# Performance work log

Measured on AMD Instinct MI355X. Metric: run time of the kernel, lower is better.

## Reference

```python
import jax, jax.numpy as jnp
import numpy as np

N, IN_DIM, HEADS, C = 100000, 128, 4, 32  # out_dim = HEADS*C = 128
E = 1600000


def setup_inputs() -> dict:
    key = jax.random.key(0)
    ks = jax.random.split(key, 9)
    x = jax.random.normal(ks[0], (N, IN_DIM), dtype=jnp.float32)
    edge_index = jax.random.randint(ks[1], (2, E), 0, N, dtype=jnp.int64)
    # GATConv params
    W = jax.random.normal(ks[2], (HEADS * C, IN_DIM), dtype=jnp.float32) * (1.0 / np.sqrt(IN_DIM))
    att_src = jax.random.normal(ks[3], (HEADS, C), dtype=jnp.float32) * 0.1
    att_dst = jax.random.normal(ks[4], (HEADS, C), dtype=jnp.float32) * 0.1
    bias = jax.random.normal(ks[5], (HEADS * C,), dtype=jnp.float32) * 0.01
    # complex phase + LayerNorm params
    phase = jax.random.normal(ks[6], (HEADS * C,), dtype=jnp.float32) * 0.02
    gamma = 1.0 + jax.random.normal(ks[7], (HEADS * C,), dtype=jnp.float32) * 0.01
    beta = jax.random.normal(ks[8], (HEADS * C,), dtype=jnp.float32) * 0.01
    return {"x": x, "edge_index": edge_index, "W": W, "att_src": att_src,
            "att_dst": att_dst, "bias": bias, "phase": phase, "gamma": gamma, "beta": beta}


def reference(x, edge_index, W, att_src, att_dst, bias, phase, gamma, beta):
    src, dst = edge_index[0], edge_index[1]
    h = (x @ W.T).reshape(N, HEADS, C)                      # [N,H,C]
    a_src = jnp.einsum('nhc,hc->nh', h, att_src)            # [N,H]
    a_dst = jnp.einsum('nhc,hc->nh', h, att_dst)
    e = jax.nn.leaky_relu(a_src[src] + a_dst[dst], 0.2)     # [E,H]
    # segment softmax over destination nodes (numerically stable)
    m = jax.ops.segment_max(e, dst, num_segments=N)         # [N,H]
    ex = jnp.exp(e - m[dst])
    s = jax.ops.segment_sum(ex, dst, num_segments=N)        # [N,H]
    alpha = ex / (s[dst] + 1e-16)                           # [E,H]
    msg = h[src] * alpha[:, :, None]                        # [E,H,C]
    out = jax.ops.segment_sum(msg, dst, num_segments=N).reshape(N, HEADS * C) + bias
    # complex phase magnitude: sqrt((h cos p)^2 + (h sin p)^2 + eps)
    mag = jnp.sqrt((out * jnp.cos(phase)) ** 2 + (out * jnp.sin(phase)) ** 2 + 1e-12)
    # LayerNorm
    mu = mag.mean(-1, keepdims=True)
    var = ((mag - mu) ** 2).mean(-1, keepdims=True)
    hn = (mag - mu) / jnp.sqrt(var + 1e-5) * gamma + beta
    return jax.nn.gelu(hn, approximate=False)
```

## Files before the change

kernel.cpp:

```cpp
#include <hip/hip_runtime.h>
#include <hip/hip_bf16.h>

#define N_ 100000
#define E_ 1600000
#define D_ 128
#define H_ 4
#define C_ 32
#define XSTR 136
#define NSCAT 256
#define E_CHUNK 6250
#define PARTS 782
#define NP 128
#define EBUF 2560
#define NLIN 512
#define FLAT (PARTS * NSCAT)
#define SCB 196

using bf16 = __hip_bfloat16;
typedef __attribute__((ext_vector_type(8))) short short8;
typedef __attribute__((ext_vector_type(4))) float f32x4;
typedef __attribute__((ext_vector_type(2))) float f32x2;

__device__ __forceinline__ float u2f(unsigned u) { return __uint_as_float(u); }
__device__ __forceinline__ unsigned short f2bu(float v) {
  bf16 t = __float2bfloat16(v);
  return *(unsigned short*)&t;
}

__global__ __launch_bounds__(256) void k_linear_histo(
    const float* __restrict__ x, const float* __restrict__ W,
    const float* __restrict__ att_src, const float* __restrict__ att_dst,
    const int* __restrict__ ei, int* __restrict__ count,
    bf16* __restrict__ h, float* __restrict__ a_src, float* __restrict__ a_dst) {
  __shared__ unsigned short WB[16384];
  __shared__ unsigned short XS[64 * XSTR];
  __shared__ float ats[128], atd[128];
  const int tid = threadIdx.x;
  const int bid = blockIdx.x;

  if (bid >= NLIN) {
    int* hist = (int*)WB;
    const int b = bid - NLIN;
    for (int i = tid; i < PARTS; i += 256) hist[i] = 0;
    __syncthreads();
    const int base = b * E_CHUNK;
    for (int i = tid; i < E_CHUNK; i += 256)
      atomicAdd(&hist[ei[E_ + base + i] >> 7], 1);
    __syncthreads();
    for (int p = tid; p < PARTS; p += 256) count[p * NSCAT + b] = hist[p];
    return;
  }

  const int lb = bid;
  const int lane = tid & 63, w = tid >> 6;
  const int n15 = lane & 15, quad = lane >> 4;

  for (int i = tid; i < 16384; i += 256) {
    const int n = i >> 7, k = i & 127;
    const int kk = k >> 5, q = (k >> 3) & 3, j = k & 7;
    const int frag = kk * 8 + (n >> 4);
    WB[frag * 512 + q * 128 + (n & 15) * 8 + j] = f2bu(W[n * 128 + k]);
  }
  if (tid < 128) { ats[tid] = att_src[tid]; atd[tid] = att_dst[tid]; }
  __syncthreads();

  const int nrb = (N_ + 63) / 64;
  for (int rb = lb; rb < nrb; rb += NLIN) {
    const int row0 = rb * 64;
    const int arow = row0 + w * 16 + n15;

    short8 af[4];
#pragma unroll
    for (int kk = 0; kk < 4; kk++) {
      float4 p = make_float4(0.f, 0.f, 0.f, 0.f);
      float4 q = make_float4(0.f, 0.f, 0.f, 0.f);
      if (arow < N_) {
        const float* xp = &x[(size_t)arow * 128 + kk * 32 + quad * 8];
        p = *(const float4*)xp;
        q = *(const float4*)(xp + 4);
      }
      short8 a;
      a[0] = f2bu(p.x); a[1] = f2bu(p.y); a[2] = f2bu(p.z); a[3] = f2bu(p.w);
      a[4] = f2bu(q.x); a[5] = f2bu(q.y); a[6] = f2bu(q.z); a[7] = f2bu(q.w);
      af[kk] = a;
    }

    f32x4 acc[8] = {};
#pragma unroll
    for (int kk = 0; kk < 4; kk++)
#pragma unroll
      for (int t = 0; t < 8; t++) {
        const short8 bfr = *(const short8*)&WB[(kk * 8 + t) * 512 + lane * 8];
        acc[t] = __builtin_amdgcn_mfma_f32_16x16x32_bf16(af[kk], bfr, acc[t], 0, 0, 0);
      }

#pragma unroll
    for (int t = 0; t < 8; t++)
#pragma unroll
      for (int reg = 0; reg < 4; reg++)
        XS[(w * 16 + quad * 4 + reg) * XSTR + t * 16 + n15] = f2bu(acc[t][reg]);

    const int lrow = lane >> 2, hd = lane & 3, cb = hd * 32;
    const int grow = row0 + w * 16 + lrow;
    if (grow < N_) {
      float ps = 0.f, pd = 0.f;
#pragma unroll
      for (int g = 0; g < 4; g++) {
        const uint4 v = *(const uint4*)&XS[(w * 16 + lrow) * XSTR + cb + g * 8];
        *(uint4*)&h[(size_t)grow * 128 + cb + g * 8] = v;
        const unsigned uu[4] = {v.x, v.y, v.z, v.w};
#pragma unroll
        for (int p2 = 0; p2 < 4; p2++) {
          const float f0 = u2f(uu[p2] << 16);
          const float f1 = u2f(uu[p2] & 0xffff0000u);
          const int cc = cb + g * 8 + p2 * 2;
          ps = fmaf(f0, ats[cc], ps);  ps = fmaf(f1, ats[cc + 1], ps);
          pd = fmaf(f0, atd[cc], pd);  pd = fmaf(f1, atd[cc + 1], pd);
        }
      }
      a_src[grow * 4 + hd] = ps;
      a_dst[grow * 4 + hd] = pd;
    }
  }
}

__global__ __launch_bounds__(1024) void k_scanA(int* __restrict__ count,
                                                int* __restrict__ bsum) {
  __shared__ int ps[1024];
  const int g = blockIdx.x, t = threadIdx.x;
  const int idx = g * 1024 + t;
  const int v = (idx < FLAT) ? count[idx] : 0;
  ps[t] = v;
  __syncthreads();
  for (int off = 1; off < 1024; off <<= 1) {
    const int add = (t >= off) ? ps[t - off] : 0;
    __syncthreads();
    ps[t] += add;
    __syncthreads();
  }
  if (idx < FLAT) count[idx] = ps[t] - v;
  if (t == 1023) bsum[g] = ps[t];
}

__global__ __launch_bounds__(1024) void k_scanB(int* __restrict__ count,
                                                const int* __restrict__ bsum,
                                                int* __restrict__ part_ptr) {
  const int g = blockIdx.x, t = threadIdx.x;
  int off = 0;
  for (int i = 0; i < g; i++) off += bsum[i];
  const int idx = g * 1024 + t;
  if (idx < FLAT) {
    const int val = count[idx] + off;
    count[idx] = val;
    if ((idx & (NSCAT - 1)) == 0) part_ptr[idx / NSCAT] = val;
  }
  if (g == SCB - 1 && t == 1023) part_ptr[PARTS] = E_;
}

__global__ __launch_bounds__(256) void k_scatter(const int* __restrict__ ei,
                                                 const int* __restrict__ base,
                                                 int* __restrict__ eout) {
  __shared__ int lbase[PARTS];
  const int b = blockIdx.x, tid = threadIdx.x;
  for (int p = tid; p < PARTS; p += 256) lbase[p] = base[p * NSCAT + b];
  __syncthreads();
  const int ebase = b * E_CHUNK;
  for (int i = tid; i < E_CHUNK; i += 256) {
    const int e = ebase + i;
    const int s = ei[e];
    const int d = ei[E_ + e];
    const int pos = atomicAdd(&lbase[d >> 7], 1);
    eout[pos] = s | ((d & 127) << 20);
  }
}

__global__ __launch_bounds__(256) void k_sortw(
    const int* __restrict__ part_ptr, int* __restrict__ eout,
    const float* __restrict__ a_src, const float* __restrict__ a_dst,
    float* __restrict__ ew, int* __restrict__ nodeptr, int* __restrict__ degN) {
  __shared__ int ebuf[EBUF];
  __shared__ int lsrc[EBUF];
  __shared__ int lcnt[NP], loff[NP], lptr[NP], ls[NP];
  const int p = blockIdx.x, tid = threadIdx.x;
  const int lo = part_ptr[p];
  int ne = part_ptr[p + 1] - lo;
  if (ne > EBUF) ne = EBUF;

  for (int i = tid; i < ne; i += 256) ebuf[i] = eout[lo + i];
  for (int n = tid; n < NP; n += 256) { lcnt[n] = 0; loff[n] = 0; }
  __syncthreads();
  for (int i = tid; i < ne; i += 256) atomicAdd(&lcnt[ebuf[i] >> 20], 1);
  __syncthreads();
  if (tid < NP) ls[tid] = lcnt[tid];
  __syncthreads();
  for (int off = 1; off < NP; off <<= 1) {
    const int v = (tid < NP && tid >= off) ? ls[tid - off] : 0;
    __syncthreads();
    if (tid < NP) ls[tid] += v;
    __syncthreads();
  }
  if (tid < NP) lptr[tid] = ls[tid] - lcnt[tid];
  __syncthreads();
  for (int i = tid; i < ne; i += 256) {
    const int v = ebuf[i];
    const int n = v >> 20;
    const int s = v & 0x1FFFF;
    const int off = atomicAdd(&loff[n], 1);
    const int pos = lptr[n] + off;
    lsrc[pos] = s;
    const int d = p * NP + n;
    const float4 asv = *(const float4*)&a_src[s * 4];
    const float4 adv = *(const float4*)&a_dst[d * 4];
    float e0 = asv.x + adv.x; e0 = (e0 > 0.f) ? e0 : 0.2f * e0;
    float e1 = asv.y + adv.y; e1 = (e1 > 0.f) ? e1 : 0.2f * e1;
    float e2 = asv.z + adv.z; e2 = (e2 > 0.f) ? e2 : 0.2f * e2;
    float e3 = asv.w + adv.w; e3 = (e3 > 0.f) ? e3 : 0.2f * e3;
    float4 wv;
    wv.x = __expf(e0); wv.y = __expf(e1); wv.z = __expf(e2); wv.w = __expf(e3);
    *(float4*)&ew[(size_t)(lo + pos) * 4] = wv;
  }
  __syncthreads();
  for (int i = tid; i < ne; i += 256) eout[lo + i] = lsrc[i];
  if (tid < NP) {
    const int g = p * NP + tid;
    if (g < N_) { nodeptr[g] = lo + lptr[tid]; degN[g] = lcnt[tid]; }
  }
}

__global__ __launch_bounds__(256) void k_gather(
    const int* __restrict__ nodeptr, const int* __restrict__ degN,
    const int* __restrict__ srcsorted, const float* __restrict__ ew,
    const bf16* __restrict__ h, const float* __restrict__ bias,
    const float* __restrict__ gamma, const float* __restrict__ beta,
    float* __restrict__ out) {
  const int lane = threadIdx.x & 63;
  const int d = blockIdx.x * 4 + (threadIdx.x >> 6);
  if (d >= N_) return;
  const int head = lane >> 4;
  const int ch = lane * 2;
  const int deg0 = degN[d];
  const int deg = deg0 < 64 ? deg0 : 64;
  const int ptr = nodeptr[d];
  const float* __restrict__ ewp = ew + (size_t)ptr * 4;

  int my_src = 0;
  if (lane < deg) my_src = srcsorted[ptr + lane];

  float acc0 = 0.f, acc1 = 0.f, sumw = 0.f;

  int j = 0;
  for (; j + 4 <= deg; j += 4) {
    const int s0 = __builtin_amdgcn_readlane(my_src, j);
    const int s1 = __builtin_amdgcn_readlane(my_src, j + 1);
    const int s2 = __builtin_amdgcn_readlane(my_src, j + 2);
    const int s3 = __builtin_amdgcn_readlane(my_src, j + 3);
    const float w0 = ewp[(j + 0) * 4 + head];
    const float w1 = ewp[(j + 1) * 4 + head];
    const float w2 = ewp[(j + 2) * 4 + head];
    const float w3 = ewp[(j + 3) * 4 + head];
    const unsigned h0 = *(const unsigned*)&h[((size_t)s0 << 7) + ch];
    const unsigned h1 = *(const unsigned*)&h[((size_t)s1 << 7) + ch];
    const unsigned h2 = *(const unsigned*)&h[((size_t)s2 << 7) + ch];
    const unsigned h3 = *(const unsigned*)&h[((size_t)s3 << 7) + ch];
    sumw += w0 + w1 + w2 + w3;
    acc0 = fmaf(w0, u2f(h0 << 16), acc0); acc1 = fmaf(w0, u2f(h0 & 0xffff0000u), acc1);
    acc0 = fmaf(w1, u2f(h1 << 16), acc0); acc1 = fmaf(w1, u2f(h1 & 0xffff0000u), acc1);
    acc0 = fmaf(w2, u2f(h2 << 16), acc0); acc1 = fmaf(w2, u2f(h2 & 0xffff0000u), acc1);
    acc0 = fmaf(w3, u2f(h3 << 16), acc0); acc1 = fmaf(w3, u2f(h3 & 0xffff0000u), acc1);
  }
  for (; j < deg; ++j) {
    const int s = __builtin_amdgcn_readlane(my_src, j);
    const float wv = ewp[j * 4 + head];
    const unsigned hv = *(const unsigned*)&h[((size_t)s << 7) + ch];
    sumw += wv;
    acc0 = fmaf(wv, u2f(hv << 16), acc0);
    acc1 = fmaf(wv, u2f(hv & 0xffff0000u), acc1);
  }

  const float inv = 1.0f / (sumw + 1e-16f);
  const float2 bi = *(const float2*)&bias[ch];
  const float v0 = acc0 * inv + bi.x;
  const float v1 = acc1 * inv + bi.y;
  const float m0i = sqrtf(v0 * v0 + 1e-12f);
  const float m1i = sqrtf(v1 * v1 + 1e-12f);

  float s1r = m0i + m1i;
#pragma unroll
  for (int off = 32; off > 0; off >>= 1) s1r += __shfl_xor(s1r, off);
  const float mu = s1r * (1.0f / 128.0f);
  const float d0 = m0i - mu, d1 = m1i - mu;
  float q = d0 * d0 + d1 * d1;
#pragma unroll
  for (int off = 32; off > 0; off >>= 1) q += __shfl_xor(q, off);
  const float rstd = rsqrtf(q * (1.0f / 128.0f) + 1e-5f);
  const float2 ga = *(const float2*)&gamma[ch];
  const float2 be = *(const float2*)&beta[ch];
  const float hn0 = d0 * rstd * ga.x + be.x;
  const float hn1 = d1 * rstd * ga.y + be.y;
  const float g0 = 0.5f * hn0 * (1.0f + erff(hn0 * 0.70710678118654752f));
  const float g1 = 0.5f * hn1 * (1.0f + erff(hn1 * 0.70710678118654752f));
  f32x2 gv; gv.x = g0; gv.y = g1;
  __builtin_nontemporal_store(gv, (f32x2*)&out[(size_t)d * 128 + ch]);
}

extern "C" void kernel_launch(void* const* d_in, const int* in_sizes, int n_in,
                              void* d_out, int out_size, void* d_ws, size_t ws_size,
                              hipStream_t stream) {
  const float* x       = (const float*)d_in[0];
  const int*   ei      = (const int*)d_in[1];
  const float* W       = (const float*)d_in[2];
  const float* att_src = (const float*)d_in[3];
  const float* att_dst = (const float*)d_in[4];
  const float* bias    = (const float*)d_in[5];
  const float* gamma   = (const float*)d_in[7];
  const float* beta    = (const float*)d_in[8];
  float* out = (float*)d_out;

  bf16*  h        = (bf16*)d_ws;
  float* a_src    = (float*)(h + (size_t)N_ * D_);
  float* a_dst    = a_src + (size_t)N_ * H_;
  int*   count    = (int*)(a_dst + (size_t)N_ * H_);
  int*   bsum     = count + (size_t)FLAT;
  int*   part_ptr = bsum + 256;
  int*   eout     = part_ptr + 800;
  float* ew       = (float*)(eout + (size_t)E_);
  int*   nodeptr  = (int*)(ew + (size_t)E_ * 4);
  int*   degN     = nodeptr + (size_t)N_;

  k_linear_histo<<<NLIN + NSCAT, 256, 0, stream>>>(x, W, att_src, att_dst, ei,
                                                   count, h, a_src, a_dst);
  k_scanA<<<SCB, 1024, 0, stream>>>(count, bsum);
  k_scanB<<<SCB, 1024, 0, stream>>>(count, bsum, part_ptr);
  k_scatter<<<NSCAT, 256, 0, stream>>>(ei, count, eout);
  k_sortw<<<PARTS, 256, 0, stream>>>(part_ptr, eout, a_src, a_dst, ew,
                                     nodeptr, degN);
  k_gather<<<(N_ + 3) / 4, 256, 0, stream>>>(nodeptr, degN, eout, ew, h,
                                             bias, gamma, beta, out);
}
```

Before: 279.7 us.

## Split linear projection across histogram, scan and scatter kernels to overlap work

The dense x@W projection was previously done entirely alongside the histogram kernel. It is now split into four row ranges, each run by extra blocks inside the histogram, scanA, scanB and scatter launches, so the small sort-preparation kernels share the machine with matmul work. The scan kernels also move from 1024-thread blocks to 256-thread blocks that each handle 4 elements. The cost is that every launch now reserves the large shared-memory footprint and reloads W into shared memory, and the load balance depends on the chosen row split.

```diff
diff --git a/kernel.cpp b/kernel.cpp
--- a/kernel.cpp
+++ b/kernel.cpp
@@ -12,9 +12,12 @@
 #define PARTS 782
 #define NP 128
 #define EBUF 2560
-#define NLIN 512
 #define FLAT (PARTS * NSCAT)
-#define SCB 196
+#define NSC 196
+#define RB1 300
+#define RB2 400
+#define RB3 500
+#define NRB 1563
 
 using bf16 = __hip_bfloat16;
 typedef __attribute__((ext_vector_type(8))) short short8;
@@ -27,31 +30,12 @@
   return *(unsigned short*)&t;
 }
 
-__global__ __launch_bounds__(256) void k_linear_histo(
+__device__ __forceinline__ void linear_body(
+    unsigned short* WB, unsigned short* XS, float* ats, float* atd,
     const float* __restrict__ x, const float* __restrict__ W,
     const float* __restrict__ att_src, const float* __restrict__ att_dst,
-    const int* __restrict__ ei, int* __restrict__ count,
-    bf16* __restrict__ h, float* __restrict__ a_src, float* __restrict__ a_dst) {
-  __shared__ unsigned short WB[16384];
-  __shared__ unsigned short XS[64 * XSTR];
-  __shared__ float ats[128], atd[128];
-  const int tid = threadIdx.x;
-  const int bid = blockIdx.x;
-
-  if (bid >= NLIN) {
-    int* hist = (int*)WB;
-    const int b = bid - NLIN;
-    for (int i = tid; i < PARTS; i += 256) hist[i] = 0;
-    __syncthreads();
-    const int base = b * E_CHUNK;
-    for (int i = tid; i < E_CHUNK; i += 256)
-      atomicAdd(&hist[ei[E_ + base + i] >> 7], 1);
-    __syncthreads();
-    for (int p = tid; p < PARTS; p += 256) count[p * NSCAT + b] = hist[p];
-    return;
-  }
-
-  const int lb = bid;
+    bf16* __restrict__ h, float* __restrict__ a_src, float* __restrict__ a_dst,
+    int lb, int nlin, int rb0, int rb1, int tid) {
   const int lane = tid & 63, w = tid >> 6;
   const int n15 = lane & 15, quad = lane >> 4;
 
@@ -64,8 +48,7 @@
   if (tid < 128) { ats[tid] = att_src[tid]; atd[tid] = att_dst[tid]; }
   __syncthreads();
 
-  const int nrb = (N_ + 63) / 64;
-  for (int rb = lb; rb < nrb; rb += NLIN) {
+  for (int rb = rb0 + lb; rb < rb1; rb += nlin) {
     const int row0 = rb * 64;
     const int arow = row0 + w * 16 + n15;
 
@@ -124,54 +107,128 @@
   }
 }
 
-__global__ __launch_bounds__(1024) void k_scanA(int* __restrict__ count,
-                                                int* __restrict__ bsum) {
-  __shared__ int ps[1024];
-  const int g = blockIdx.x, t = threadIdx.x;
-  const int idx = g * 1024 + t;
-  const int v = (idx < FLAT) ? count[idx] : 0;
-  ps[t] = v;
-  __syncthreads();
-  for (int off = 1; off < 1024; off <<= 1) {
-    const int add = (t >= off) ? ps[t - off] : 0;
-    __syncthreads();
-    ps[t] += add;
-    __syncthreads();
-  }
-  if (idx < FLAT) count[idx] = ps[t] - v;
-  if (t == 1023) bsum[g] = ps[t];
-}
-
-__global__ __launch_bounds__(1024) void k_scanB(int* __restrict__ count,
-                                                const int* __restrict__ bsum,
-                                                int* __restrict__ part_ptr) {
-  const int g = blockIdx.x, t = threadIdx.x;
-  int off = 0;
-  for (int i = 0; i < g; i++) off += bsum[i];
-  const int idx = g * 1024 + t;
-  if (idx < FLAT) {
-    const int val = count[idx] + off;
-    count[idx] = val;
-    if ((idx & (NSCAT - 1)) == 0) part_ptr[idx / NSCAT] = val;
-  }
-  if (g == SCB - 1 && t == 1023) part_ptr[PARTS] = E_;
-}
-
-__global__ __launch_bounds__(256) void k_scatter(const int* __restrict__ ei,
-                                                 const int* __restrict__ base,
-                                                 int* __restrict__ eout) {
-  __shared__ int lbase[PARTS];
-  const int b = blockIdx.x, tid = threadIdx.x;
-  for (int p = tid; p < PARTS; p += 256) lbase[p] = base[p * NSCAT + b];
-  __syncthreads();
-  const int ebase = b * E_CHUNK;
-  for (int i = tid; i < E_CHUNK; i += 256) {
-    const int e = ebase + i;
-    const int s = ei[e];
-    const int d = ei[E_ + e];
-    const int pos = atomicAdd(&lbase[d >> 7], 1);
-    eout[pos] = s | ((d & 127) << 20);
-  }
+__global__ __launch_bounds__(256) void k1_histo_lin(
+    const float* __restrict__ x, const float* __restrict__ W,
+    const float* __restrict__ att_src, const float* __restrict__ att_dst,
+    const int* __restrict__ ei, int* __restrict__ count,
+    bf16* __restrict__ h, float* __restrict__ a_src, float* __restrict__ a_dst) {
+  __shared__ unsigned short WB[16384];
+  __shared__ unsigned short XS[64 * XSTR];
+  __shared__ float ats[128], atd[128];
+  const int tid = threadIdx.x, bid = blockIdx.x;
+
+  if (bid < NSCAT) {
+    int* hist = (int*)WB;
+    for (int i = tid; i < PARTS; i += 256) hist[i] = 0;
+    __syncthreads();
+    const int base = bid * E_CHUNK;
+    for (int i = tid; i < E_CHUNK; i += 256)
+      atomicAdd(&hist[ei[E_ + base + i] >> 7], 1);
+    __syncthreads();
+    for (int p = tid; p < PARTS; p += 256) count[p * NSCAT + bid] = hist[p];
+    return;
+  }
+  linear_body(WB, XS, ats, atd, x, W, att_src, att_dst, h, a_src, a_dst,
+              bid - NSCAT, 512, 0, RB1, tid);
+}
+
+__global__ __launch_bounds__(256) void k2_scanA_lin(
+    const float* __restrict__ x, const float* __restrict__ W,
+    const float* __restrict__ att_src, const float* __restrict__ att_dst,
+    int* __restrict__ count, int* __restrict__ bsum,
+    bf16* __restrict__ h, float* __restrict__ a_src, float* __restrict__ a_dst) {
+  __shared__ unsigned short WB[16384];
+  __shared__ unsigned short XS[64 * XSTR];
+  __shared__ float ats[128], atd[128];
+  __shared__ int ts[256];
+  const int tid = threadIdx.x, bid = blockIdx.x;
+
+  if (bid < NSC) {
+    const int i0 = bid * 1024 + tid * 4;
+    int v0 = 0, v1 = 0, v2 = 0, v3 = 0;
+    if (i0 < FLAT)     v0 = count[i0];
+    if (i0 + 1 < FLAT) v1 = count[i0 + 1];
+    if (i0 + 2 < FLAT) v2 = count[i0 + 2];
+    if (i0 + 3 < FLAT) v3 = count[i0 + 3];
+    const int s = v0 + v1 + v2 + v3;
+    ts[tid] = s;
+    __syncthreads();
+    for (int off = 1; off < 256; off <<= 1) {
+      const int add = (tid >= off) ? ts[tid - off] : 0;
+      __syncthreads();
+      ts[tid] += add;
+      __syncthreads();
+    }
+    const int excl = ts[tid] - s;
+    if (i0 < FLAT)     count[i0]     = excl;
+    if (i0 + 1 < FLAT) count[i0 + 1] = excl + v0;
+    if (i0 + 2 < FLAT) count[i0 + 2] = excl + v0 + v1;
+    if (i0 + 3 < FLAT) count[i0 + 3] = excl + v0 + v1 + v2;
+    if (tid == 255) bsum[bid] = ts[255];
+    return;
+  }
+  linear_body(WB, XS, ats, atd, x, W, att_src, att_dst, h, a_src, a_dst,
+              bid - NSC, 572, RB1, RB2, tid);
+}
+
+__global__ __launch_bounds__(256) void k3_scanB_lin(
+    const float* __restrict__ x, const float* __restrict__ W,
+    const float* __restrict__ att_src, const float* __restrict__ att_dst,
+    int* __restrict__ count, const int* __restrict__ bsum,
+    int* __restrict__ part_ptr,
+    bf16* __restrict__ h, float* __restrict__ a_src, float* __restrict__ a_dst) {
+  __shared__ unsigned short WB[16384];
+  __shared__ unsigned short XS[64 * XSTR];
+  __shared__ float ats[128], atd[128];
+  const int tid = threadIdx.x, bid = blockIdx.x;
+
+  if (bid < NSC) {
+    int off = 0;
+    for (int i = 0; i < bid; i++) off += bsum[i];
+    const int i0 = bid * 1024 + tid * 4;
+#pragma unroll
+    for (int k = 0; k < 4; k++) {
+      const int idx = i0 + k;
+      if (idx < FLAT) {
+        const int val = count[idx] + off;
+        count[idx] = val;
+        if ((idx & (NSCAT - 1)) == 0) part_ptr[idx >> 8] = val;
+      }
+    }
+    if (bid == 0 && tid == 0) part_ptr[PARTS] = E_;
+    return;
+  }
+  linear_body(WB, XS, ats, atd, x, W, att_src, att_dst, h, a_src, a_dst,
+              bid - NSC, 572, RB2, RB3, tid);
+}
+
+__global__ __launch_bounds__(256) void k4_scatter_lin(
+    const float* __restrict__ x, const float* __restrict__ W,
+    const float* __restrict__ att_src, const float* __restrict__ att_dst,
+    const int* __restrict__ ei, const int* __restrict__ base,
+    int* __restrict__ eout,
+    bf16* __restrict__ h, float* __restrict__ a_src, float* __restrict__ a_dst) {
+  __shared__ unsigned short WB[16384];
+  __shared__ unsigned short XS[64 * XSTR];
+  __shared__ float ats[128], atd[128];
+  const int tid = threadIdx.x, bid = blockIdx.x;
+
+  if (bid < NSCAT) {
+    int* lbase = (int*)WB;
+    for (int p = tid; p < PARTS; p += 256) lbase[p] = base[p * NSCAT + bid];
+    __syncthreads();
+    const int ebase = bid * E_CHUNK;
+    for (int i = tid; i < E_CHUNK; i += 256) {
+      const int e = ebase + i;
+      const int s = ei[e];
+      const int d = ei[E_ + e];
+      const int pos = atomicAdd(&lbase[d >> 7], 1);
+      eout[pos] = s | ((d & 127) << 20);
+    }
+    return;
+  }
+  linear_body(WB, XS, ats, atd, x, W, att_src, att_dst, h, a_src, a_dst,
+              bid - NSCAT, 512, RB3, NRB, tid);
 }
 
 __global__ __launch_bounds__(256) void k_sortw(
@@ -327,11 +384,15 @@
   int*   nodeptr  = (int*)(ew + (size_t)E_ * 4);
   int*   degN     = nodeptr + (size_t)N_;
 
-  k_linear_histo<<<NLIN + NSCAT, 256, 0, stream>>>(x, W, att_src, att_dst, ei,
-                                                   count, h, a_src, a_dst);
-  k_scanA<<<SCB, 1024, 0, stream>>>(count, bsum);
-  k_scanB<<<SCB, 1024, 0, stream>>>(count, bsum, part_ptr);
-  k_scatter<<<NSCAT, 256, 0, stream>>>(ei, count, eout);
+  k1_histo_lin<<<NSCAT + 512, 256, 0, stream>>>(x, W, att_src, att_dst, ei,
+                                                count, h, a_src, a_dst);
+  k2_scanA_lin<<<NSC + 572, 256, 0, stream>>>(x, W, att_src, att_dst,
+                                              count, bsum, h, a_src, a_dst);
+  k3_scanB_lin<<<NSC + 572, 256, 0, stream>>>(x, W, att_src, att_dst,
+                                              count, bsum, part_ptr,
+                                              h, a_src, a_dst);
+  k4_scatter_lin<<<NSCAT + 512, 256, 0, stream>>>(x, W, att_src, att_dst, ei,
+                                                  count, eout, h, a_src, a_dst);
   k_sortw<<<PARTS, 256, 0, stream>>>(part_ptr, eout, a_src, a_dst, ew,
                                      nodeptr, degN);
   k_gather<<<(N_ + 3) / 4, 256, 0, stream>>>(nodeptr, degN, eout, ew, h,
```

New measurement: 286.0 us. +2.3%, slower.
